# Kernel tuning notes

Hardware: AMD Instinct MI355X
Metric: run time of the kernel (lower is better)

The kernel has to match this reference:

```python
import jax, jax.numpy as jnp
import numpy as np

NU, NI, E = 200000, 100000, 500000
D, H, O = 128, 256, 128  # embedding_dim, hidden_dim, output_dim


def _sage(x_src, x_dst, src, dst, n_dst, W_l, b_l, W_r):
    """PyG SAGEConv (mean aggr): lin_l(mean_j x_src[j]) + lin_r(x_dst)."""
    msgs = x_src[src]                                            # [E, d_in]
    summed = jax.ops.segment_sum(msgs, dst, num_segments=n_dst)  # [n_dst, d_in]
    deg = jax.ops.segment_sum(jnp.ones(src.shape, x_src.dtype), dst, num_segments=n_dst)
    mean = summed / jnp.maximum(deg, 1.0)[:, None]
    return mean @ W_l + b_l + x_dst @ W_r


def setup_inputs() -> dict:
    key = jax.random.key(0)
    ks = jax.random.split(key, 18)

    def w(k, i, o):
        return jax.random.normal(k, (i, o), jnp.float32) / np.float32(np.sqrt(i))

    return {
        "x_user": jax.random.normal(ks[0], (NU, D), jnp.float32),
        "x_item": jax.random.normal(ks[1], (NI, D), jnp.float32),
        "edge_src": jax.random.randint(ks[2], (E,), 0, NU, jnp.int32),
        "edge_dst": jax.random.randint(ks[3], (E,), 0, NI, jnp.int32),
        # layer 1 (encoder): D -> H, one SAGEConv per edge type
        "W_l1_ui": w(ks[4], D, H), "W_r1_ui": w(ks[5], D, H), "b_l1_ui": jnp.zeros((H,), jnp.float32),
        "W_l1_iu": w(ks[6], D, H), "W_r1_iu": w(ks[7], D, H), "b_l1_iu": jnp.zeros((H,), jnp.float32),
        # layer 2 (projection): H -> O
        "W_l2_ui": w(ks[8], H, O), "W_r2_ui": w(ks[9], H, O), "b_l2_ui": jnp.zeros((O,), jnp.float32),
        "W_l2_iu": w(ks[10], H, O), "W_r2_iu": w(ks[11], H, O), "b_l2_iu": jnp.zeros((O,), jnp.float32),
    }


def reference(x_user, x_item, edge_src, edge_dst,
              W_l1_ui, W_r1_ui, b_l1_ui, W_l1_iu, W_r1_iu, b_l1_iu,
              W_l2_ui, W_r2_ui, b_l2_ui, W_l2_iu, W_r2_iu, b_l2_iu):
    # encoder layer: relu(SAGEConv) per destination node type (dropout=eval/no-op)
    h_item = jax.nn.relu(_sage(x_user, x_item, edge_src, edge_dst, NI, W_l1_ui, b_l1_ui, W_r1_ui))
    h_user = jax.nn.relu(_sage(x_item, x_user, edge_dst, edge_src, NU, W_l1_iu, b_l1_iu, W_r1_iu))
    # extra relu in RecommendationGNN.forward is a no-op after relu
    # projection layer: relu(SAGEConv), dropout=0
    o_item = jax.nn.relu(_sage(h_user, h_item, edge_src, edge_dst, NI, W_l2_ui, b_l2_ui, W_r2_ui))
    o_user = jax.nn.relu(_sage(h_item, h_user, edge_dst, edge_src, NU, W_l2_iu, b_l2_iu, W_r2_iu))
    return (o_user, o_item)
```

## Files before the change

kernel.cpp:

```cpp
#include <hip/hip_runtime.h>
#include <stdint.h>

typedef __attribute__((ext_vector_type(8))) short short8;
typedef __attribute__((ext_vector_type(4))) float f32x4;

#define SCAN_TILE 4096

__device__ __forceinline__ float bf2f(unsigned short u) {
  union { unsigned int i; float f; } v;
  v.i = ((unsigned int)u) << 16;
  return v.f;
}
__device__ __forceinline__ unsigned short f2bf(float f) {
  union { float f; unsigned int i; } v;
  v.f = f;
  unsigned int u = v.i;
  return (unsigned short)((u + 0x7FFFu + ((u >> 16) & 1u)) >> 16);
}
__device__ __forceinline__ unsigned int pack2(float a, float b) {
  return (unsigned int)f2bf(a) | ((unsigned int)f2bf(b) << 16);
}
__device__ __forceinline__ void add2(float& a, float& b, unsigned int v) {
  a += bf2f((unsigned short)(v & 0xffff));
  b += bf2f((unsigned short)(v >> 16));
}

__device__ __forceinline__ size_t fragS128(int row, int k) {
  return ((size_t)(row >> 4) * 4 + (size_t)(k >> 5)) * 512
       + (size_t)((((row & 15) + (((k >> 3) & 3) << 4)) << 3) + (k & 7));
}

__global__ __launch_bounds__(256) void build_wt_all(
    const float* __restrict__ Wl1ui, const float* __restrict__ Wr1ui,
    const float* __restrict__ Wl1iu, const float* __restrict__ Wr1iu,
    const float* __restrict__ Wl2ui, const float* __restrict__ Wr2ui,
    const float* __restrict__ Wl2iu, const float* __restrict__ Wr2iu,
    unsigned short* __restrict__ T1ui_l, unsigned short* __restrict__ T1ui_h,
    unsigned short* __restrict__ T1iu_l, unsigned short* __restrict__ T1iu_h,
    unsigned short* __restrict__ T2lui_l, unsigned short* __restrict__ T2lui_h,
    unsigned short* __restrict__ T2rui_l, unsigned short* __restrict__ T2rui_h,
    unsigned short* __restrict__ T2liu_l, unsigned short* __restrict__ T2liu_h,
    unsigned short* __restrict__ T2riu_l, unsigned short* __restrict__ T2riu_h)
{
  int idx = blockIdx.x * 256 + threadIdx.x;
  const float *W1, *W2;
  unsigned short *lo, *hi;
  int N, rel;
  if (idx < 65536)       { W1 = Wl1ui; W2 = Wr1ui;          lo = T1ui_l;  hi = T1ui_h;  N = 256; rel = idx; }
  else if (idx < 131072) { W1 = Wl1iu; W2 = Wr1iu;          lo = T1iu_l;  hi = T1iu_h;  N = 256; rel = idx - 65536; }
  else if (idx < 163840) { W1 = Wl2ui; W2 = Wl2ui + 128*128; lo = T2lui_l; hi = T2lui_h; N = 128; rel = idx - 131072; }
  else if (idx < 196608) { W1 = Wr2ui; W2 = Wr2ui + 128*128; lo = T2rui_l; hi = T2rui_h; N = 128; rel = idx - 163840; }
  else if (idx < 229376) { W1 = Wl2iu; W2 = Wl2iu + 128*128; lo = T2liu_l; hi = T2liu_h; N = 128; rel = idx - 196608; }
  else                   { W1 = Wr2iu; W2 = Wr2iu + 128*128; lo = T2riu_l; hi = T2riu_h; N = 128; rel = idx - 229376; }
  int n = rel >> 8;
  int k = rel & 255;
  float v = (k < 128) ? W1[(size_t)k * N + n] : W2[(size_t)(k - 128) * N + n];
  if (k < 128) lo[fragS128(n, k)] = f2bf(v);
  else         hi[fragS128(n, k - 128)] = f2bf(v);
}

__global__ __launch_bounds__(256) void conv_x(
    const float* __restrict__ xu, const float* __restrict__ xi,
    uint4* __restrict__ XfI, uint4* __restrict__ XfU,
    int NI, int NU, int MI, int MU)
{
  int u = blockIdx.x * 256 + threadIdx.x;
  int unitsI = MI * 16;
  const float* x; uint4* Xf; int M; int rel;
  if (u < unitsI) { x = xi; Xf = XfI; M = NI; rel = u; }
  else {
    rel = u - unitsI;
    if (rel >= MU * 16) return;
    x = xu; Xf = XfU; M = NU;
  }
  int c = rel >> 6;
  int s = rel & 63;
  int row = ((c >> 2) << 4) + (s & 15);
  int k = ((c & 3) << 5) + ((s >> 4) << 3);
  uint4 o = make_uint4(0u, 0u, 0u, 0u);
  if (row < M) {
    f32x4 a = *(const f32x4*)(x + (size_t)row * 128 + k);
    f32x4 b = *(const f32x4*)(x + (size_t)row * 128 + k + 4);
    o.x = pack2(a[0], a[1]); o.y = pack2(a[2], a[3]);
    o.z = pack2(b[0], b[1]); o.w = pack2(b[2], b[3]);
  }
  Xf[rel] = o;
}

__global__ __launch_bounds__(256) void hist(
    const int* __restrict__ esrc, const int* __restrict__ edst,
    int* __restrict__ cntAll, int NI, int E)
{
  int e = blockIdx.x * 256 + threadIdx.x;
  if (e >= E) return;
  atomicAdd(&cntAll[edst[e]], 1);
  atomicAdd(&cntAll[NI + esrc[e]], 1);
}

__global__ __launch_bounds__(256) void scan_p1(
    const int* __restrict__ cnt, int* __restrict__ tileSums, int NA)
{
  __shared__ int red[256];
  int b = blockIdx.x, t = threadIdx.x;
  int base = b * SCAN_TILE;
  int s = 0;
  for (int i = t; i < SCAN_TILE; i += 256) {
    int g = base + i;
    if (g < NA) s += cnt[g];
  }
  red[t] = s;
  __syncthreads();
  for (int d = 128; d > 0; d >>= 1) {
    if (t < d) red[t] += red[t + d];
    __syncthreads();
  }
  if (t == 0) tileSums[b] = red[0];
}

__global__ __launch_bounds__(256) void scan_p2(
    int* __restrict__ tileSums, int nTiles, int* __restrict__ offEnd)
{
  __shared__ int buf[256];
  int t = threadIdx.x;
  int v = (t < nTiles) ? tileSums[t] : 0;
  buf[t] = v;
  __syncthreads();
  for (int d = 1; d < 256; d <<= 1) {
    int x = (t >= d) ? buf[t - d] : 0;
    __syncthreads();
    buf[t] += x;
    __syncthreads();
  }
  if (t < nTiles) tileSums[t] = buf[t] - v;
  if (t == nTiles - 1) *offEnd = buf[t];
}

__global__ __launch_bounds__(256) void scan_p3(
    const int* __restrict__ cnt, const int* __restrict__ tileSums,
    int* __restrict__ off, int NA)
{
  __shared__ int red[256];
  int b = blockIdx.x, t = threadIdx.x;
  int base = b * SCAN_TILE + t * 16;
  int loc[16];
  int s = 0;
#pragma unroll
  for (int i = 0; i < 16; ++i) {
    int g = base + i;
    loc[i] = (g < NA) ? cnt[g] : 0;
    s += loc[i];
  }
  red[t] = s;
  __syncthreads();
  for (int d = 1; d < 256; d <<= 1) {
    int x = (t >= d) ? red[t - d] : 0;
    __syncthreads();
    red[t] += x;
    __syncthreads();
  }
  int run = tileSums[b] + red[t] - s;
#pragma unroll
  for (int i = 0; i < 16; ++i) {
    int g = base + i;
    if (g < NA) off[g] = run;
    run += loc[i];
  }
}

__global__ __launch_bounds__(256) void fill_idx(
    const int* __restrict__ esrc, const int* __restrict__ edst,
    const int* __restrict__ offAll, int* __restrict__ curAll,
    int* __restrict__ idxAll, int NI, int E)
{
  int e = blockIdx.x * 256 + threadIdx.x;
  if (e >= E) return;
  int s = esrc[e], d = edst[e];
  int pI = offAll[d] + atomicAdd(&curAll[d], 1);
  idxAll[pI] = s;
  int pU = offAll[NI + s] + atomicAdd(&curAll[NI + s], 1);
  idxAll[pU] = d;
}

__global__ __launch_bounds__(256) void build_mean(
    const float* __restrict__ xu, const float* __restrict__ xi,
    const int* __restrict__ idxAll, const int* __restrict__ offAll,
    unsigned short* __restrict__ MfI, unsigned short* __restrict__ MfU,
    int NI, int NA)
{
  int w2 = (blockIdx.x * 256 + threadIdx.x) >> 6;
  int l = threadIdx.x & 63;
  int h = l >> 5;
  int lh = l & 31;
  int node = w2 * 2 + h;
  if (node >= NA) return;
  bool isItem = (node < NI);
  const float* xo = isItem ? xu : xi;
  unsigned short* Mf = isItem ? MfI : MfU;
  int n = isItem ? node : (node - NI);
  int s = offAll[node], e = offAll[node + 1];

  f32x4 acc = (f32x4){0.f, 0.f, 0.f, 0.f};
  int j = s;
  for (; j + 1 < e; j += 2) {
    int g0 = idxAll[j];
    int g1 = idxAll[j + 1];
    f32x4 v0 = *(const f32x4*)(xo + (size_t)g0 * 128 + lh * 4);
    f32x4 v1 = *(const f32x4*)(xo + (size_t)g1 * 128 + lh * 4);
    acc += v0 + v1;
  }
  if (j < e) {
    int g = idxAll[j];
    acc += *(const f32x4*)(xo + (size_t)g * 128 + lh * 4);
  }

  float inv = 1.0f / (float)max(e - s, 1);
  uint2 o;
  o.x = pack2(acc[0] * inv, acc[1] * inv);
  o.y = pack2(acc[2] * inv, acc[3] * inv);
  *(uint2*)(Mf + fragS128(n, lh * 4)) = o;
}

__global__ __launch_bounds__(256) void seg_mean(
    const unsigned int* __restrict__ pU, const unsigned int* __restrict__ pI,
    const int* __restrict__ idxAll, const int* __restrict__ offAll,
    unsigned int* __restrict__ m2I, unsigned int* __restrict__ m2U,
    int NI, int NA)
{
  int w4 = (blockIdx.x * 256 + threadIdx.x) >> 6;
  int l = threadIdx.x & 63;
  int q = l >> 4;
  int lq = l & 15;
  int node = w4 * 4 + q;
  if (node >= NA) return;
  bool isItem = (node < NI);
  const unsigned int* p = isItem ? pU : pI;
  unsigned int* m2 = isItem ? m2I : m2U;
  int n = isItem ? node : (node - NI);
  int s = offAll[node], e = offAll[node + 1];

  float a0 = 0.f, a1 = 0.f, a2 = 0.f, a3 = 0.f,
        a4 = 0.f, a5 = 0.f, a6 = 0.f, a7 = 0.f;

  int j = s;
  for (; j + 1 < e; j += 2) {
    int g0 = idxAll[j];
    int g1 = idxAll[j + 1];
    uint4 v0 = *(const uint4*)(p + (size_t)g0 * 64 + lq * 4);
    uint4 v1 = *(const uint4*)(p + (size_t)g1 * 64 + lq * 4);
    add2(a0, a1, v0.x); add2(a2, a3, v0.y); add2(a4, a5, v0.z); add2(a6, a7, v0.w);
    add2(a0, a1, v1.x); add2(a2, a3, v1.y); add2(a4, a5, v1.z); add2(a6, a7, v1.w);
  }
  if (j < e) {
    int g = idxAll[j];
    uint4 v = *(const uint4*)(p + (size_t)g * 64 + lq * 4);
    add2(a0, a1, v.x); add2(a2, a3, v.y); add2(a4, a5, v.z); add2(a6, a7, v.w);
  }

  float inv = 1.0f / (float)max(e - s, 1);
  uint4 o;
  o.x = pack2(a0 * inv, a1 * inv);
  o.y = pack2(a2 * inv, a3 * inv);
  o.z = pack2(a4 * inv, a5 * inv);
  o.w = pack2(a6 * inv, a7 * inv);
  *(uint4*)(m2 + (size_t)n * 64 + lq * 4) = o;
}

struct GemmP {
  const unsigned short* Alo; const unsigned short* Ahi;
  const unsigned short* Blo; const unsigned short* Bhi;
  const float* bias;
  const unsigned short* Madd;
  void* outp; unsigned short* outHi;
  int M;
};

__global__ __launch_bounds__(256, 4) void gemm_flat(
    GemmP P0, GemmP P1, int rb0,
    int outF32, int outFrag, int N, int doRelu)
{
  __shared__ uint4 lB[2048];

  const int bx = blockIdx.x;
  const bool first = (bx < rb0);
  GemmP P = first ? P0 : P1;
  const int mb = first ? bx : bx - rb0;

  const int tid = threadIdx.x;
  const int lane = tid & 63;
  const int wave = tid >> 6;
  const int m0 = mb * 128 + (wave >> 1) * 64;
  const int nBase = blockIdx.y * 128;
  const int n0 = nBase + (wave & 1) * 64;
  const int r16 = lane & 15;
  const int quad = lane >> 4;
  const int cgl = (wave & 1) * 4;

  const uint4* AL = (const uint4*)P.Alo;
  const uint4* AH = (const uint4*)P.Ahi;
  const uint4* BL = (const uint4*)P.Blo + (size_t)(nBase >> 4) * 256;
  const uint4* BH = (const uint4*)P.Bhi + (size_t)(nBase >> 4) * 256;
  const size_t aB = (size_t)(m0 >> 4) * 256 + lane;

  f32x4 acc[4][4];
#pragma unroll
  for (int i = 0; i < 4; ++i)
#pragma unroll
    for (int j = 0; j < 4; ++j) acc[i][j] = (f32x4){0.f, 0.f, 0.f, 0.f};

  short8 avp[4];
#pragma unroll
  for (int g = 0; g < 4; ++g) {
    uint4 t = AL[aB + (size_t)(g * 4) * 64];
    avp[g] = *(const short8*)&t;
  }
#pragma unroll
  for (int i = 0; i < 8; ++i)
    lB[i * 256 + tid] = BL[i * 256 + tid];
  __syncthreads();

#pragma unroll
  for (int k0 = 0; k0 < 4; ++k0) {
    short8 av[4], bv[4];
#pragma unroll
    for (int g = 0; g < 4; ++g) {
      if (k0 == 0) av[g] = avp[g];
      else {
        uint4 t = AL[aB + (size_t)(g * 4 + k0) * 64];
        av[g] = *(const short8*)&t;
      }
      uint4 tb = lB[((cgl + g) * 4 + k0) * 64 + lane];
      bv[g] = *(const short8*)&tb;
    }
#pragma unroll
    for (int mg = 0; mg < 4; ++mg)
#pragma unroll
      for (int ng = 0; ng < 4; ++ng)
        acc[mg][ng] = __builtin_amdgcn_mfma_f32_16x16x32_bf16(bv[ng], av[mg], acc[mg][ng], 0, 0, 0);
  }
  __syncthreads();

#pragma unroll
  for (int g = 0; g < 4; ++g) {
    uint4 t = AH[aB + (size_t)(g * 4) * 64];
    avp[g] = *(const short8*)&t;
  }
#pragma unroll
  for (int i = 0; i < 8; ++i)
    lB[i * 256 + tid] = BH[i * 256 + tid];
  __syncthreads();

#pragma unroll
  for (int k0 = 0; k0 < 4; ++k0) {
    short8 av[4], bv[4];
#pragma unroll
    for (int g = 0; g < 4; ++g) {
      if (k0 == 0) av[g] = avp[g];
      else {
        uint4 t = AH[aB + (size_t)(g * 4 + k0) * 64];
        av[g] = *(const short8*)&t;
      }
      uint4 tb = lB[((cgl + g) * 4 + k0) * 64 + lane];
      bv[g] = *(const short8*)&tb;
    }
#pragma unroll
    for (int mg = 0; mg < 4; ++mg)
#pragma unroll
      for (int ng = 0; ng < 4; ++ng)
        acc[mg][ng] = __builtin_amdgcn_mfma_f32_16x16x32_bf16(bv[ng], av[mg], acc[mg][ng], 0, 0, 0);
  }

#pragma unroll
  for (int mg = 0; mg < 4; ++mg) {
    int row = m0 + mg * 16 + r16;
    if (row < P.M) {
#pragma unroll
      for (int ng = 0; ng < 4; ++ng) {
        int col = n0 + ng * 16 + quad * 4;
        f32x4 v = acc[mg][ng];
        if (P.bias) {
          f32x4 b4 = *(const f32x4*)(P.bias + col);
          v += b4;
        }
        if (P.Madd) {
          uint2 md = *(const uint2*)(P.Madd + (size_t)row * 128 + col);
          v[0] += bf2f((unsigned short)(md.x & 0xffff));
          v[1] += bf2f((unsigned short)(md.x >> 16));
          v[2] += bf2f((unsigned short)(md.y & 0xffff));
          v[3] += bf2f((unsigned short)(md.y >> 16));
        }
        if (doRelu) {
          v[0] = fmaxf(v[0], 0.0f); v[1] = fmaxf(v[1], 0.0f);
          v[2] = fmaxf(v[2], 0.0f); v[3] = fmaxf(v[3], 0.0f);
        }
        if (outF32) {
          *(f32x4*)((float*)P.outp + (size_t)row * N + col) = v;
        } else {
          uint2 o;
          o.x = pack2(v[0], v[1]);
          o.y = pack2(v[2], v[3]);
          if (outFrag) {
            if (col < 128) *(uint2*)((unsigned short*)P.outp + fragS128(row, col)) = o;
            else           *(uint2*)(P.outHi + fragS128(row, col - 128)) = o;
          } else {
            *(uint2*)((unsigned short*)P.outp + (size_t)row * N + col) = o;
          }
        }
      }
    }
  }
}

extern "C" void kernel_launch(void* const* d_in, const int* in_sizes, int n_in,
                              void* d_out, int out_size, void* d_ws, size_t ws_size,
                              hipStream_t stream)
{
  const float* x_user  = (const float*)d_in[0];
  const float* x_item  = (const float*)d_in[1];
  const int*   esrc    = (const int*)d_in[2];
  const int*   edst    = (const int*)d_in[3];
  const float* W_l1_ui = (const float*)d_in[4];
  const float* W_r1_ui = (const float*)d_in[5];
  const float* b_l1_ui = (const float*)d_in[6];
  const float* W_l1_iu = (const float*)d_in[7];
  const float* W_r1_iu = (const float*)d_in[8];
  const float* b_l1_iu = (const float*)d_in[9];
  const float* W_l2_ui = (const float*)d_in[10];
  const float* W_r2_ui = (const float*)d_in[11];
  const float* b_l2_ui = (const float*)d_in[12];
  const float* W_l2_iu = (const float*)d_in[13];
  const float* W_r2_iu = (const float*)d_in[14];
  const float* b_l2_iu = (const float*)d_in[15];

  const int NU = in_sizes[0] / 128;
  const int NI = in_sizes[1] / 128;
  const int E  = in_sizes[2];
  const int NA = NI + NU;
  const int MI = ((NI + 127) / 128) * 128;
  const int MU = ((NU + 127) / 128) * 128;

  char* ws = (char*)d_ws;
  size_t off = 0;
  auto alloc = [&](size_t bytes) -> void* {
    void* p = ws + off;
    off += (bytes + 255) & ~(size_t)255;
    return p;
  };

  int* cntAll = (int*)alloc((size_t)NA * 4);
  int* curAll = (int*)alloc((size_t)NA * 4);
  size_t zeroBytes = off;
  int* offAll   = (int*)alloc((size_t)(NA + 1) * 4);
  int* tileSums = (int*)alloc(256 * 4);
  int* idxAll   = (int*)alloc((size_t)2 * E * 4);
  unsigned short* T1ui_l  = (unsigned short*)alloc(256 * 128 * 2);
  unsigned short* T1ui_h  = (unsigned short*)alloc(256 * 128 * 2);
  unsigned short* T1iu_l  = (unsigned short*)alloc(256 * 128 * 2);
  unsigned short* T1iu_h  = (unsigned short*)alloc(256 * 128 * 2);
  unsigned short* T2lui_l = (unsigned short*)alloc(128 * 128 * 2);
  unsigned short* T2lui_h = (unsigned short*)alloc(128 * 128 * 2);
  unsigned short* T2rui_l = (unsigned short*)alloc(128 * 128 * 2);
  unsigned short* T2rui_h = (unsigned short*)alloc(128 * 128 * 2);
  unsigned short* T2liu_l = (unsigned short*)alloc(128 * 128 * 2);
  unsigned short* T2liu_h = (unsigned short*)alloc(128 * 128 * 2);
  unsigned short* T2riu_l = (unsigned short*)alloc(128 * 128 * 2);
  unsigned short* T2riu_h = (unsigned short*)alloc(128 * 128 * 2);
  unsigned short* h_item = (unsigned short*)alloc((size_t)MI * 256 * 2);
  unsigned short* h_item_hi = h_item + (size_t)MI * 128;
  unsigned short* h_user = (unsigned short*)alloc((size_t)MU * 256 * 2);
  unsigned short* h_user_hi = h_user + (size_t)MU * 128;
  char* R = (char*)alloc((size_t)(MI + MU) * 256 * 2);
  unsigned short* Mf_item = (unsigned short*)R;
  unsigned short* Mf_user = (unsigned short*)(R + (size_t)MI * 128 * 2);
  unsigned short* Xf_item = (unsigned short*)(R + (size_t)(MI + MU) * 128 * 2);
  unsigned short* Xf_user = (unsigned short*)(R + (size_t)(2 * MI + MU) * 128 * 2);
  unsigned short* p_user = (unsigned short*)R;
  unsigned short* p_item = (unsigned short*)(R + (size_t)NU * 128 * 2);
  unsigned short* m2I    = (unsigned short*)(R + (size_t)(NU + NI) * 128 * 2);
  unsigned short* m2U    = (unsigned short*)(R + (size_t)(NU + 2 * NI) * 128 * 2);

  float* out = (float*)d_out;

  hipMemsetAsync(ws, 0, zeroBytes, stream);

  build_wt_all<<<1024, 256, 0, stream>>>(
      W_l1_ui, W_r1_ui, W_l1_iu, W_r1_iu, W_l2_ui, W_r2_ui, W_l2_iu, W_r2_iu,
      T1ui_l, T1ui_h, T1iu_l, T1iu_h,
      T2lui_l, T2lui_h, T2rui_l, T2rui_h, T2liu_l, T2liu_h, T2riu_l, T2riu_h);

  int units = (MI + MU) * 16;
  conv_x<<<(units + 255) / 256, 256, 0, stream>>>(
      x_user, x_item, (uint4*)Xf_item, (uint4*)Xf_user, NI, NU, MI, MU);

  int egrid = (E + 255) / 256;
  int nTiles = (NA + SCAN_TILE - 1) / SCAN_TILE;
  hist<<<egrid, 256, 0, stream>>>(esrc, edst, cntAll, NI, E);
  scan_p1<<<nTiles, 256, 0, stream>>>(cntAll, tileSums, NA);
  scan_p2<<<1, 256, 0, stream>>>(tileSums, nTiles, offAll + NA);
  scan_p3<<<nTiles, 256, 0, stream>>>(cntAll, tileSums, offAll, NA);
  fill_idx<<<egrid, 256, 0, stream>>>(esrc, edst, offAll, curAll, idxAll, NI, E);

  int waves1 = (NA + 1) / 2;
  build_mean<<<(waves1 * 64 + 255) / 256, 256, 0, stream>>>(
      x_user, x_item, idxAll, offAll, Mf_item, Mf_user, NI, NA);

  const int rbI = MI / 128, rbU = MU / 128;

  GemmP l1i = {Mf_item, Xf_item, T1ui_l, T1ui_h, b_l1_ui, nullptr, h_item, h_item_hi, NI};
  GemmP l1u = {Mf_user, Xf_user, T1iu_l, T1iu_h, b_l1_iu, nullptr, h_user, h_user_hi, NU};
  gemm_flat<<<dim3(rbI + rbU, 2), 256, 0, stream>>>(l1i, l1u, rbI, 0, 1, 256, 1);

  GemmP pi = {h_item, h_item_hi, T2liu_l, T2liu_h, nullptr, nullptr, p_item, nullptr, NI};
  GemmP pu = {h_user, h_user_hi, T2lui_l, T2lui_h, nullptr, nullptr, p_user, nullptr, NU};
  gemm_flat<<<dim3(rbI + rbU, 1), 256, 0, stream>>>(pi, pu, rbI, 0, 0, 128, 0);

  int waves2 = (NA + 3) / 4;
  seg_mean<<<(waves2 * 64 + 255) / 256, 256, 0, stream>>>(
      (const unsigned int*)p_user, (const unsigned int*)p_item,
      idxAll, offAll, (unsigned int*)m2I, (unsigned int*)m2U, NI, NA);

  GemmP oi = {h_item, h_item_hi, T2rui_l, T2rui_h, b_l2_ui, m2I,
              out + (size_t)NU * 128, nullptr, NI};
  GemmP ou = {h_user, h_user_hi, T2riu_l, T2riu_h, b_l2_iu, m2U,
              out, nullptr, NU};
  gemm_flat<<<dim3(rbI + rbU, 1), 256, 0, stream>>>(oi, ou, rbI, 1, 0, 128, 1);
}
```

Measured before the change: 869.4 us.

## Prefetch all A fragments into registers and double-buffer B in LDS for gemm

The GEMM kernel now issues every global load for the lo and hi A fragments up front into registers, and stages the hi half of B into a second LDS buffer. This removes one barrier and the serial load-then-compute phases. The aim is to hide global memory latency behind the MFMA work. In exchange, register use and LDS size double, so launch bounds drop from 4 to 2 blocks per CU, which lowers occupancy.

Result: faster. 815.7 us (-6.2%).

```diff
diff --git a/kernel.cpp b/kernel.cpp
--- a/kernel.cpp
+++ b/kernel.cpp
@@ -274,11 +274,11 @@
   int M;
 };
 
-__global__ __launch_bounds__(256, 4) void gemm_flat(
+__global__ __launch_bounds__(256, 2) void gemm_flat(
     GemmP P0, GemmP P1, int rb0,
     int outF32, int outFrag, int N, int doRelu)
 {
-  __shared__ uint4 lB[2048];
+  __shared__ uint4 lB[4096];
 
   const int bx = blockIdx.x;
   const bool first = (bx < rb0);
@@ -301,72 +301,73 @@
   const uint4* BH = (const uint4*)P.Bhi + (size_t)(nBase >> 4) * 256;
   const size_t aB = (size_t)(m0 >> 4) * 256 + lane;
 
+  uint4 bs[8];
+#pragma unroll
+  for (int i = 0; i < 8; ++i) bs[i] = BL[i * 256 + tid];
+
+  uint4 alo[16];
+#pragma unroll
+  for (int k0 = 0; k0 < 4; ++k0)
+#pragma unroll
+    for (int g = 0; g < 4; ++g)
+      alo[k0 * 4 + g] = AL[aB + (size_t)(g * 256 + k0 * 64)];
+
+#pragma unroll
+  for (int i = 0; i < 8; ++i) lB[i * 256 + tid] = bs[i];
+
+  uint4 ahi[16];
+#pragma unroll
+  for (int k0 = 0; k0 < 4; ++k0)
+#pragma unroll
+    for (int g = 0; g < 4; ++g)
+      ahi[k0 * 4 + g] = AH[aB + (size_t)(g * 256 + k0 * 64)];
+
+  asm volatile("s_waitcnt lgkmcnt(0)\ns_barrier" ::: "memory");
+
   f32x4 acc[4][4];
 #pragma unroll
   for (int i = 0; i < 4; ++i)
 #pragma unroll
     for (int j = 0; j < 4; ++j) acc[i][j] = (f32x4){0.f, 0.f, 0.f, 0.f};
 
-  short8 avp[4];
-#pragma unroll
-  for (int g = 0; g < 4; ++g) {
-    uint4 t = AL[aB + (size_t)(g * 4) * 64];
-    avp[g] = *(const short8*)&t;
-  }
-#pragma unroll
-  for (int i = 0; i < 8; ++i)
-    lB[i * 256 + tid] = BL[i * 256 + tid];
-  __syncthreads();
-
 #pragma unroll
   for (int k0 = 0; k0 < 4; ++k0) {
-    short8 av[4], bv[4];
+    short8 bv[4];
 #pragma unroll
     for (int g = 0; g < 4; ++g) {
-      if (k0 == 0) av[g] = avp[g];
-      else {
-        uint4 t = AL[aB + (size_t)(g * 4 + k0) * 64];
-        av[g] = *(const short8*)&t;
-      }
       uint4 tb = lB[((cgl + g) * 4 + k0) * 64 + lane];
       bv[g] = *(const short8*)&tb;
     }
 #pragma unroll
-    for (int mg = 0; mg < 4; ++mg)
+    for (int mg = 0; mg < 4; ++mg) {
+      short8 av = *(const short8*)&alo[k0 * 4 + mg];
 #pragma unroll
       for (int ng = 0; ng < 4; ++ng)
-        acc[mg][ng] = __builtin_amdgcn_mfma_f32_16x16x32_bf16(bv[ng], av[mg], acc[mg][ng], 0, 0, 0);
-  }
-  __syncthreads();
-
-#pragma unroll
-  for (int g = 0; g < 4; ++g) {
-    uint4 t = AH[aB + (size_t)(g * 4) * 64];
-    avp[g] = *(const short8*)&t;
-  }
-#pragma unroll
-  for (int i = 0; i < 8; ++i)
-    lB[i * 256 + tid] = BH[i * 256 + tid];
-  __syncthreads();
+        acc[mg][ng] = __builtin_amdgcn_mfma_f32_16x16x32_bf16(bv[ng], av, acc[mg][ng], 0, 0, 0);
+    }
+  }
+
+#pragma unroll
+  for (int i = 0; i < 8; ++i) bs[i] = BH[i * 256 + tid];
+#pragma unroll
+  for (int i = 0; i < 8; ++i) lB[2048 + i * 256 + tid] = bs[i];
+  asm volatile("s_waitcnt lgkmcnt(0)\ns_barrier" ::: "memory");
 
 #pragma unroll
   for (int k0 = 0; k0 < 4; ++k0) {
-    short8 av[4], bv[4];
+    short8 bv[4];
 #pragma unroll
     for (int g = 0; g < 4; ++g) {
-      if (k0 == 0) av[g] = avp[g];
-      else {
-        uint4 t = AH[aB + (size_t)(g * 4 + k0) * 64];
-        av[g] = *(const short8*)&t;
-      }
-      uint4 tb = lB[((cgl + g) * 4 + k0) * 64 + lane];
+      uint4 tb = lB[2048 + ((cgl + g) * 4 + k0) * 64 + lane];
       bv[g] = *(const short8*)&tb;
     }
 #pragma unroll
-    for (int mg = 0; mg < 4; ++mg)
+    for (int mg = 0; mg < 4; ++mg) {
+      short8 av = *(const short8*)&ahi[k0 * 4 + mg];
 #pragma unroll
       for (int ng = 0; ng < 4; ++ng)
-        acc[mg][ng] = __builtin_amdgcn_mfma_f32_16x16x32_bf16(bv[ng], av[mg], acc[mg][ng], 0, 0, 0);
+        acc[mg][ng] = __builtin_amdgcn_mfma_f32_16x16x32_bf16(bv[ng], av, acc[mg][ng], 0, 0, 0);
+    }
   }
 
 #pragma unroll
```

## Pipeline GEMM operand loads via direct global-to-LDS double buffering

Applied to the files above, without the earlier changes.

Replaces the GEMM main loop's per-wave direct global A loads and the staged B copy into shared memory with asynchronous global_load_lds transfers of both A and B tiles. Two LDS buffers are filled one k-stage ahead, with manual vmcnt and barrier waits, so memory traffic can overlap the MFMA work. The launch_bounds occupancy hint is also dropped. This trades simpler code for hand-written waitcnt and barrier logic, and A is now read through LDS instead of straight into registers.

Result: faster. 828.7 us (-4.7%).

```diff
diff --git a/kernel.cpp b/kernel.cpp
--- a/kernel.cpp
+++ b/kernel.cpp
@@ -274,11 +274,11 @@
   int M;
 };
 
-__global__ __launch_bounds__(256, 4) void gemm_flat(
+__global__ __launch_bounds__(256) void gemm_flat(
     GemmP P0, GemmP P1, int rb0,
     int outF32, int outFrag, int N, int doRelu)
 {
-  __shared__ uint4 lB[2048];
+  __shared__ __attribute__((aligned(16))) uint4 lds4[2048];
 
   const int bx = blockIdx.x;
   const bool first = (bx < rb0);
@@ -288,18 +288,38 @@
   const int tid = threadIdx.x;
   const int lane = tid & 63;
   const int wave = tid >> 6;
-  const int m0 = mb * 128 + (wave >> 1) * 64;
   const int nBase = blockIdx.y * 128;
-  const int n0 = nBase + (wave & 1) * 64;
   const int r16 = lane & 15;
   const int quad = lane >> 4;
-  const int cgl = (wave & 1) * 4;
 
   const uint4* AL = (const uint4*)P.Alo;
   const uint4* AH = (const uint4*)P.Ahi;
   const uint4* BL = (const uint4*)P.Blo + (size_t)(nBase >> 4) * 256;
   const uint4* BH = (const uint4*)P.Bhi + (size_t)(nBase >> 4) * 256;
-  const size_t aB = (size_t)(m0 >> 4) * 256 + lane;
+
+  const int fa = wave * 2;
+
+#define STAGE(s, b) do {                                                        \
+    const uint4* As_ = ((s) < 4 ? AL : AH);                                     \
+    const uint4* Bs_ = ((s) < 4 ? BL : BH);                                     \
+    const int k0_ = (s) & 3;                                                    \
+    const uint4* ga0 = As_ + ((size_t)((mb * 8 + fa) * 4 + k0_)) * 64 + lane;   \
+    const uint4* ga1 = As_ + ((size_t)((mb * 8 + fa + 1) * 4 + k0_)) * 64 + lane;\
+    const uint4* gb0 = Bs_ + ((size_t)(fa * 4 + k0_)) * 64 + lane;              \
+    const uint4* gb1 = Bs_ + ((size_t)((fa + 1) * 4 + k0_)) * 64 + lane;        \
+    __builtin_amdgcn_global_load_lds(                                           \
+        (const __attribute__((address_space(1))) void*)ga0,                     \
+        (__attribute__((address_space(3))) void*)&lds4[(b) * 1024 + fa * 64], 16, 0, 0); \
+    __builtin_amdgcn_global_load_lds(                                           \
+        (const __attribute__((address_space(1))) void*)ga1,                     \
+        (__attribute__((address_space(3))) void*)&lds4[(b) * 1024 + (fa + 1) * 64], 16, 0, 0); \
+    __builtin_amdgcn_global_load_lds(                                           \
+        (const __attribute__((address_space(1))) void*)gb0,                     \
+        (__attribute__((address_space(3))) void*)&lds4[(b) * 1024 + 512 + fa * 64], 16, 0, 0); \
+    __builtin_amdgcn_global_load_lds(                                           \
+        (const __attribute__((address_space(1))) void*)gb1,                     \
+        (__attribute__((address_space(3))) void*)&lds4[(b) * 1024 + 512 + (fa + 1) * 64], 16, 0, 0); \
+  } while (0)
 
   f32x4 acc[4][4];
 #pragma unroll
@@ -307,28 +327,24 @@
 #pragma unroll
     for (int j = 0; j < 4; ++j) acc[i][j] = (f32x4){0.f, 0.f, 0.f, 0.f};
 
-  short8 avp[4];
-#pragma unroll
-  for (int g = 0; g < 4; ++g) {
-    uint4 t = AL[aB + (size_t)(g * 4) * 64];
-    avp[g] = *(const short8*)&t;
-  }
-#pragma unroll
-  for (int i = 0; i < 8; ++i)
-    lB[i * 256 + tid] = BL[i * 256 + tid];
-  __syncthreads();
-
-#pragma unroll
-  for (int k0 = 0; k0 < 4; ++k0) {
+  STAGE(0, 0);
+  STAGE(1, 1);
+
+  const int wr = (wave >> 1) * 4;
+  const int wc = (wave & 1) * 4;
+
+#pragma unroll
+  for (int s = 0; s < 8; ++s) {
+    const int b = s & 1;
+    if (s < 7) asm volatile("s_waitcnt vmcnt(4)\ns_barrier" ::: "memory");
+    else       asm volatile("s_waitcnt vmcnt(0)\ns_barrier" ::: "memory");
+
     short8 av[4], bv[4];
 #pragma unroll
     for (int g = 0; g < 4; ++g) {
-      if (k0 == 0) av[g] = avp[g];
-      else {
-        uint4 t = AL[aB + (size_t)(g * 4 + k0) * 64];
-        av[g] = *(const short8*)&t;
-      }
-      uint4 tb = lB[((cgl + g) * 4 + k0) * 64 + lane];
+      uint4 ta = lds4[b * 1024 + (wr + g) * 64 + lane];
+      uint4 tb = lds4[b * 1024 + 512 + (wc + g) * 64 + lane];
+      av[g] = *(const short8*)&ta;
       bv[g] = *(const short8*)&tb;
     }
 #pragma unroll
@@ -336,39 +352,16 @@
 #pragma unroll
       for (int ng = 0; ng < 4; ++ng)
         acc[mg][ng] = __builtin_amdgcn_mfma_f32_16x16x32_bf16(bv[ng], av[mg], acc[mg][ng], 0, 0, 0);
-  }
-  __syncthreads();
-
-#pragma unroll
-  for (int g = 0; g < 4; ++g) {
-    uint4 t = AH[aB + (size_t)(g * 4) * 64];
-    avp[g] = *(const short8*)&t;
-  }
-#pragma unroll
-  for (int i = 0; i < 8; ++i)
-    lB[i * 256 + tid] = BH[i * 256 + tid];
-  __syncthreads();
-
-#pragma unroll
-  for (int k0 = 0; k0 < 4; ++k0) {
-    short8 av[4], bv[4];
-#pragma unroll
-    for (int g = 0; g < 4; ++g) {
-      if (k0 == 0) av[g] = avp[g];
-      else {
-        uint4 t = AH[aB + (size_t)(g * 4 + k0) * 64];
-        av[g] = *(const short8*)&t;
-      }
-      uint4 tb = lB[((cgl + g) * 4 + k0) * 64 + lane];
-      bv[g] = *(const short8*)&tb;
+
+    if (s < 6) {
+      asm volatile("s_waitcnt lgkmcnt(0)\ns_barrier" ::: "memory");
+      STAGE(s + 2, b);
     }
-#pragma unroll
-    for (int mg = 0; mg < 4; ++mg)
-#pragma unroll
-      for (int ng = 0; ng < 4; ++ng)
-        acc[mg][ng] = __builtin_amdgcn_mfma_f32_16x16x32_bf16(bv[ng], av[mg], acc[mg][ng], 0, 0, 0);
-  }
-
+  }
+#undef STAGE
+
+  const int m0 = mb * 128 + (wave >> 1) * 64;
+  const int n0 = nBase + (wave & 1) * 64;
 #pragma unroll
   for (int mg = 0; mg < 4; ++mg) {
     int row = m0 + mg * 16 + r16;
```
